# Optimization experiments

Hardware: AMD Instinct MI355X
Metric: run time of the kernel (lower is better)

Reference implementation:

```python
import jax, jax.numpy as jnp
import numpy as np

BS, QLEN, DIM, H = 2, 2048, 2048, 16
DH = DIM // H


def setup_inputs() -> dict:
    key = jax.random.key(0)
    ks = jax.random.split(key, 10)
    s = 0.02
    return {
        "input": jax.random.normal(ks[0], (BS, QLEN, DIM), jnp.float32),
        "mask": jnp.ones((BS, QLEN), jnp.int32),
        "wq": jax.random.normal(ks[1], (DIM, DIM), jnp.float32) * s,
        "bq": jax.random.normal(ks[2], (DIM,), jnp.float32) * s,
        "wk": jax.random.normal(ks[3], (DIM, DIM), jnp.float32) * s,
        "bk": jax.random.normal(ks[4], (DIM,), jnp.float32) * s,
        "wv": jax.random.normal(ks[5], (DIM, DIM), jnp.float32) * s,
        "bv": jax.random.normal(ks[6], (DIM,), jnp.float32) * s,
        "wo": jax.random.normal(ks[7], (DIM, DIM), jnp.float32) * s,
        "bo": jax.random.normal(ks[8], (DIM,), jnp.float32) * s,
    }


def _shape(x, bs):
    # (bs, len, dim) -> (bs, H, len, DH)
    return x.reshape(bs, -1, H, DH).transpose(0, 2, 1, 3)


def reference(input, mask, wq, bq, wk, bk, wv, bv, wo, bo):
    bs, qlen, dim = input.shape
    # torch Linear: y = x @ W.T + b
    q = _shape(input @ wq.T + bq, bs)  # (bs,H,q,dh)
    k = _shape(input @ wk.T + bk, bs)  # (bs,H,k,dh)
    v = _shape(input @ wv.T + bv, bs)  # (bs,H,k,dh)
    q = q / jnp.sqrt(jnp.asarray(DH, q.dtype))
    scores = jnp.einsum("bhqd,bhkd->bhqk", q, k)
    # mask (bs, klen): positions where mask==0 are masked with -inf
    neg = (mask == 0)[:, None, None, :]  # (bs,1,1,klen)
    scores = jnp.where(neg, -jnp.inf, scores)
    weights = jax.nn.softmax(scores.astype(jnp.float32), axis=-1).astype(scores.dtype)
    # dropout p=0 (eval): identity
    context = jnp.einsum("bhqk,bhkd->bhqd", weights, v)
    context = context.transpose(0, 2, 1, 3).reshape(bs, qlen, dim)
    return context @ wo.T + bo
```

## Files before the change

### kernel.cpp

```cpp
#include <hip/hip_runtime.h>
#include <hip/hip_bf16.h>

#define BS 2
#define QLEN 2048
#define DIM 2048
#define H 16
#define DH 128
#define MTOT (BS*QLEN)

typedef __hip_bfloat16 bf16;
using f32x4 = __attribute__((ext_vector_type(4))) float;
using s16x8 = __attribute__((ext_vector_type(8))) short;

__device__ inline void gload_lds16(const bf16* g, bf16* l) {
    __builtin_amdgcn_global_load_lds(
        (const __attribute__((address_space(1))) void*)g,
        (__attribute__((address_space(3))) void*)l,
        16, 0, 0);
}

__global__ __launch_bounds__(256) void cast6(
    const float* __restrict__ x,
    const float* __restrict__ w0, const float* __restrict__ w1,
    const float* __restrict__ w2, const float* __restrict__ w3,
    bf16* xo, bf16* o0, bf16* o1, bf16* o2, bf16* o3, int n4)
{
    const float* in; bf16* out;
    switch (blockIdx.y) {
        case 0:  in = w0; out = o0; break;
        case 1:  in = w1; out = o1; break;
        case 2:  in = w2; out = o2; break;
        case 3:  in = w3; out = o3; break;
        case 4:  in = x;        out = xo;        break;
        default: in = x + 4*(size_t)n4; out = xo + 4*(size_t)n4; break;
    }
    int i = blockIdx.x * 256 + threadIdx.x;
    if (i < n4) {
        float4 v = ((const float4*)in)[i];
        __hip_bfloat162 p0 = __float22bfloat162_rn(make_float2(v.x, v.y));
        __hip_bfloat162 p1 = __float22bfloat162_rn(make_float2(v.z, v.w));
        ((__hip_bfloat162*)out)[2*i]   = p0;
        ((__hip_bfloat162*)out)[2*i+1] = p1;
    }
}

__global__ __launch_bounds__(256) void gemm_qkv(
    const bf16* __restrict__ A,
    const bf16* __restrict__ Wq, const bf16* __restrict__ Wk, const bf16* __restrict__ Wv,
    const float* __restrict__ bq, const float* __restrict__ bk, const float* __restrict__ bv,
    bf16* __restrict__ Qo, bf16* __restrict__ Ko, bf16* __restrict__ Vo,
    float qscale)
{
    __shared__ __align__(16) bf16 smem[128*136];
    bf16* As = smem;
    bf16* Bs = smem + 128*64;

    const int z = blockIdx.z;
    const bf16*  B    = (z == 0) ? Wq : (z == 1) ? Wk : Wv;
    const float* bias = (z == 0) ? bq : (z == 1) ? bk : bv;
    const float  scale = (z == 0) ? qscale : 1.0f;

    const int t = threadIdx.x;
    const int lane = t & 63, w = t >> 6;
    const int row16 = lane & 15, quad = lane >> 4;
    const int m0 = blockIdx.y * 128, n0 = blockIdx.x * 128;
    const int mo = (w >> 1) * 64, no = (w & 1) * 64;

    f32x4 acc[4][4];
    for (int i = 0; i < 4; i++)
        for (int j = 0; j < 4; j++)
            acc[i][j] = (f32x4){0.f, 0.f, 0.f, 0.f};

    for (int kt = 0; kt < DIM; kt += 64) {
        __syncthreads();
        #pragma unroll
        for (int i = 0; i < 4; i++) {
            int idx = i*256 + t;
            int row = idx >> 3, g = idx & 7;
            int src = g ^ (row & 7);
            gload_lds16(A + (size_t)(m0 + row) * DIM + kt + src*8, &As[idx*8]);
            gload_lds16(B + (size_t)(n0 + row) * DIM + kt + src*8, &Bs[idx*8]);
        }
        __syncthreads();

        #pragma unroll
        for (int kh = 0; kh < 2; kh++) {
            s16x8 af[4], bfr[4];
            #pragma unroll
            for (int mt = 0; mt < 4; mt++)
                af[mt] = *(const s16x8*)&As[(mo + mt*16 + row16)*64 + (((kh*4+quad) ^ (row16&7)))*8];
            #pragma unroll
            for (int nt = 0; nt < 4; nt++)
                bfr[nt] = *(const s16x8*)&Bs[(no + nt*16 + row16)*64 + (((kh*4+quad) ^ (row16&7)))*8];
            #pragma unroll
            for (int mt = 0; mt < 4; mt++)
                #pragma unroll
                for (int nt = 0; nt < 4; nt++)
                    acc[mt][nt] = __builtin_amdgcn_mfma_f32_16x16x32_bf16(
                        af[mt], bfr[nt], acc[mt][nt], 0, 0, 0);
        }
    }

    if (z < 2) {
        bf16* out = (z == 0) ? Qo : Ko;
        for (int mt = 0; mt < 4; mt++)
            for (int nt = 0; nt < 4; nt++) {
                int n = n0 + no + nt*16 + row16;
                float bv_ = bias[n];
                for (int r = 0; r < 4; r++) {
                    int m = m0 + mo + mt*16 + quad*4 + r;
                    out[(size_t)m * DIM + n] = __float2bfloat16((acc[mt][nt][r] + bv_) * scale);
                }
            }
    } else {
        __syncthreads();
        bf16* Ts = smem;
        for (int mt = 0; mt < 4; mt++)
            for (int nt = 0; nt < 4; nt++) {
                int nn = no + nt*16 + row16;
                float bv_ = bias[n0 + nn];
                for (int r = 0; r < 4; r++) {
                    int mm = mo + mt*16 + quad*4 + r;
                    Ts[nn*136 + mm] = __float2bfloat16(acc[mt][nt][r] + bv_);
                }
            }
        __syncthreads();
        const int b = m0 >> 11, q0b = m0 & 2047;
        for (int i = 0; i < 8; i++) {
            int chunk = t + i*256;
            int row = chunk >> 4;
            int c16 = chunk & 15;
            s16x8 val = *(const s16x8*)&Ts[row*136 + c16*8];
            *(s16x8*)(Vo + ((size_t)(b*DIM + n0 + row))*QLEN + q0b + c16*8) = val;
        }
    }
}

__global__ __launch_bounds__(256) void gemm_out(
    const bf16* __restrict__ A, const bf16* __restrict__ B,
    const float* __restrict__ bias, float* __restrict__ out)
{
    __shared__ __align__(16) bf16 As[128*64];
    __shared__ __align__(16) bf16 Bs[128*64];

    const int t = threadIdx.x;
    const int lane = t & 63, w = t >> 6;
    const int row16 = lane & 15, quad = lane >> 4;
    const int m0 = blockIdx.y * 128, n0 = blockIdx.x * 128;
    const int mo = (w >> 1) * 64, no = (w & 1) * 64;

    f32x4 acc[4][4];
    for (int i = 0; i < 4; i++)
        for (int j = 0; j < 4; j++)
            acc[i][j] = (f32x4){0.f, 0.f, 0.f, 0.f};

    for (int kt = 0; kt < DIM; kt += 64) {
        __syncthreads();
        #pragma unroll
        for (int i = 0; i < 4; i++) {
            int idx = i*256 + t;
            int row = idx >> 3, g = idx & 7;
            int src = g ^ (row & 7);
            gload_lds16(A + (size_t)(m0 + row) * DIM + kt + src*8, &As[idx*8]);
            gload_lds16(B + (size_t)(n0 + row) * DIM + kt + src*8, &Bs[idx*8]);
        }
        __syncthreads();

        #pragma unroll
        for (int kh = 0; kh < 2; kh++) {
            s16x8 af[4], bfr[4];
            #pragma unroll
            for (int mt = 0; mt < 4; mt++)
                af[mt] = *(const s16x8*)&As[(mo + mt*16 + row16)*64 + (((kh*4+quad) ^ (row16&7)))*8];
            #pragma unroll
            for (int nt = 0; nt < 4; nt++)
                bfr[nt] = *(const s16x8*)&Bs[(no + nt*16 + row16)*64 + (((kh*4+quad) ^ (row16&7)))*8];
            #pragma unroll
            for (int mt = 0; mt < 4; mt++)
                #pragma unroll
                for (int nt = 0; nt < 4; nt++)
                    acc[mt][nt] = __builtin_amdgcn_mfma_f32_16x16x32_bf16(
                        af[mt], bfr[nt], acc[mt][nt], 0, 0, 0);
        }
    }

    for (int mt = 0; mt < 4; mt++)
        for (int nt = 0; nt < 4; nt++) {
            int n = n0 + no + nt*16 + row16;
            float bv_ = bias[n];
            for (int r = 0; r < 4; r++) {
                int m = m0 + mo + mt*16 + quad*4 + r;
                out[(size_t)m * DIM + n] = acc[mt][nt][r] + bv_;
            }
        }
}

__global__ __launch_bounds__(256, 2) void attn(
    const bf16* __restrict__ Q, const bf16* __restrict__ Kb,
    const bf16* __restrict__ Vt, const int* __restrict__ mask,
    bf16* __restrict__ Ctx)
{
    __shared__ __align__(16) bf16 Ks[2][64*128];
    __shared__ __align__(16) bf16 Vs[128*64];
    __shared__ __align__(16) bf16 Pl[4][32*64];

    const int t = threadIdx.x, w = t >> 6, lane = t & 63;
    const int row16 = lane & 15, quad = lane >> 4;
    const int bh = blockIdx.y, b = bh >> 4, h = bh & 15;
    const int q0 = blockIdx.x * 128 + w * 32;

    s16x8 qf[2][4];
    for (int qs = 0; qs < 2; qs++) {
        const bf16* qp = Q + (size_t)(b*QLEN + q0 + qs*16 + row16) * DIM + h*DH;
        for (int ks = 0; ks < 4; ks++)
            qf[qs][ks] = *(const s16x8*)(qp + ks*32 + quad*8);
    }

    f32x4 o[2][8];
    for (int qs = 0; qs < 2; qs++)
        for (int i = 0; i < 8; i++) o[qs][i] = (f32x4){0.f, 0.f, 0.f, 0.f};
    float lsum[2][4] = {{0.f,0.f,0.f,0.f},{0.f,0.f,0.f,0.f}};
    const int* mrow = mask + b * QLEN;

    const bf16* Kbase = Kb + (size_t)b*QLEN*DIM + h*DH;
    const bf16* Vbase = Vt + ((size_t)b*DIM + h*DH) * QLEN;

    #pragma unroll
    for (int i = 0; i < 4; i++) {
        int idx = i*256 + t;
        int kr = idx >> 4, kc = idx & 15;
        int kg = kc ^ (kr & 15);
        gload_lds16(Kbase + (size_t)kr * DIM + kg*8, &Ks[0][idx*8]);
    }

    for (int it = 0; it < QLEN/64; it++) {
        const int kt = it * 64, buf = it & 1;
        __syncthreads();

        if (it + 1 < QLEN/64) {
            #pragma unroll
            for (int i = 0; i < 4; i++) {
                int idx = i*256 + t;
                int kr = idx >> 4, kc = idx & 15;
                int kg = kc ^ (kr & 15);
                gload_lds16(Kbase + (size_t)(kt + 64 + kr) * DIM + kg*8, &Ks[buf^1][idx*8]);
            }
        }
        #pragma unroll
        for (int i = 0; i < 4; i++) {
            int idx = i*256 + t;
            int vd = idx >> 3, vc = idx & 7;
            int vg = vc ^ (vd & 7);
            gload_lds16(Vbase + (size_t)vd * QLEN + kt + vg*8, &Vs[idx*8]);
        }

        float mval[4];
        #pragma unroll
        for (int nt = 0; nt < 4; nt++)
            mval[nt] = (mrow[kt + nt*16 + row16] != 0) ? -20.0f : -1e30f;

        f32x4 sc[2][4];
        for (int qs = 0; qs < 2; qs++)
            for (int nt = 0; nt < 4; nt++) sc[qs][nt] = (f32x4){0.f, 0.f, 0.f, 0.f};
        #pragma unroll
        for (int ks = 0; ks < 4; ks++) {
            #pragma unroll
            for (int nt = 0; nt < 4; nt++) {
                int rrow = nt*16 + row16;
                int c = (ks*4 + quad) ^ row16;
                s16x8 kf = *(const s16x8*)&Ks[buf][rrow*128 + c*8];
                sc[0][nt] = __builtin_amdgcn_mfma_f32_16x16x32_bf16(qf[0][ks], kf, sc[0][nt], 0, 0, 0);
                sc[1][nt] = __builtin_amdgcn_mfma_f32_16x16x32_bf16(qf[1][ks], kf, sc[1][nt], 0, 0, 0);
            }
        }

        #pragma unroll
        for (int qs = 0; qs < 2; qs++) {
            #pragma unroll
            for (int r = 0; r < 4; r++) {
                int prow = qs*16 + quad*4 + r;
                float ts = 0.f;
                #pragma unroll
                for (int nt = 0; nt < 4; nt++) {
                    float p = exp2f(sc[qs][nt][r] + mval[nt]);
                    ts += p;
                    int chunk = nt*2 + (row16 >> 3);
                    int slot = chunk ^ (prow & 7);
                    Pl[w][prow*64 + slot*8 + (row16 & 7)] = __float2bfloat16(p);
                }
                lsum[qs][r] += ts;
            }
        }

        __syncthreads();

        #pragma unroll
        for (int kc = 0; kc < 2; kc++) {
            int pslot0 = ((kc*4 + quad) ^ (row16 & 7));
            s16x8 pf0 = *(const s16x8*)&Pl[w][(0*16 + row16)*64 + pslot0*8];
            s16x8 pf1 = *(const s16x8*)&Pl[w][(1*16 + row16)*64 + pslot0*8];
            #pragma unroll
            for (int nt = 0; nt < 8; nt++) {
                int d = nt*16 + row16;
                int c = (kc*4 + quad) ^ (d & 7);
                s16x8 vf = *(const s16x8*)&Vs[d*64 + c*8];
                o[0][nt] = __builtin_amdgcn_mfma_f32_16x16x32_bf16(pf0, vf, o[0][nt], 0, 0, 0);
                o[1][nt] = __builtin_amdgcn_mfma_f32_16x16x32_bf16(pf1, vf, o[1][nt], 0, 0, 0);
            }
        }
    }

    for (int qs = 0; qs < 2; qs++) {
        float inv[4];
        for (int r = 0; r < 4; r++) {
            float ts = lsum[qs][r];
            ts += __shfl_xor(ts, 1);
            ts += __shfl_xor(ts, 2);
            ts += __shfl_xor(ts, 4);
            ts += __shfl_xor(ts, 8);
            inv[r] = 1.0f / ts;
        }
        for (int nt = 0; nt < 8; nt++)
            for (int r = 0; r < 4; r++) {
                float v = o[qs][nt][r] * inv[r];
                Ctx[(size_t)(b*QLEN + q0 + qs*16 + quad*4 + r) * DIM + h*DH + nt*16 + row16] =
                    __float2bfloat16(v);
            }
    }
}

extern "C" void kernel_launch(void* const* d_in, const int* in_sizes, int n_in,
                              void* d_out, int out_size, void* d_ws, size_t ws_size,
                              hipStream_t stream) {
    const float* x    = (const float*)d_in[0];
    const int*   mask = (const int*)d_in[1];
    const float* wq   = (const float*)d_in[2];
    const float* bq   = (const float*)d_in[3];
    const float* wk   = (const float*)d_in[4];
    const float* bk   = (const float*)d_in[5];
    const float* wv   = (const float*)d_in[6];
    const float* bv   = (const float*)d_in[7];
    const float* wo   = (const float*)d_in[8];
    const float* bo   = (const float*)d_in[9];

    char* ws = (char*)d_ws;
    const size_t MB = 1024 * 1024;
    bf16* Xb  = (bf16*)(ws);
    bf16* Qb  = (bf16*)(ws + 16*MB);
    bf16* Kb  = (bf16*)(ws + 32*MB);
    bf16* Vtb = (bf16*)(ws + 48*MB);
    bf16* Wqb = (bf16*)(ws + 64*MB);
    bf16* Wkb = (bf16*)(ws + 72*MB);
    bf16* Wvb = (bf16*)(ws + 80*MB);
    bf16* Wob = (bf16*)(ws + 88*MB);
    bf16* Ctx = Xb;

    int n4w = (DIM*DIM) / 4;
    cast6<<<dim3(n4w/256, 6), 256, 0, stream>>>(x, wq, wk, wv, wo,
                                                Xb, Wqb, Wkb, Wvb, Wob, n4w);

    const float qscale = 0.08838834764831845f * 1.4426950408889634f;
    gemm_qkv<<<dim3(DIM/128, MTOT/128, 3), 256, 0, stream>>>(
        Xb, Wqb, Wkb, Wvb, bq, bk, bv, Qb, Kb, Vtb, qscale);

    attn<<<dim3(QLEN/128, BS*H), 256, 0, stream>>>(Qb, Kb, Vtb, mask, Ctx);

    gemm_out<<<dim3(DIM/128, MTOT/128), 256, 0, stream>>>(Ctx, Wob, bo, (float*)d_out);
}
```

Baseline: 416.1 us.

## Halve attention key tile, double-buffer V, drop mid-iteration barrier

```diff
diff --git a/kernel.cpp b/kernel.cpp
--- a/kernel.cpp
+++ b/kernel.cpp
@@ -195,14 +195,14 @@
         }
 }
 
-__global__ __launch_bounds__(256, 2) void attn(
+__global__ __launch_bounds__(256, 3) void attn(
     const bf16* __restrict__ Q, const bf16* __restrict__ Kb,
     const bf16* __restrict__ Vt, const int* __restrict__ mask,
     bf16* __restrict__ Ctx)
 {
-    __shared__ __align__(16) bf16 Ks[2][64*128];
-    __shared__ __align__(16) bf16 Vs[128*64];
-    __shared__ __align__(16) bf16 Pl[4][32*64];
+    __shared__ __align__(16) bf16 Ks[2][32*128];
+    __shared__ __align__(16) bf16 Vs[2][128*32];
+    __shared__ __align__(16) bf16 Pl[4][32*32];
 
     const int t = threadIdx.x, w = t >> 6, lane = t & 63;
     const int row16 = lane & 15, quad = lane >> 4;
@@ -226,49 +226,47 @@
     const bf16* Vbase = Vt + ((size_t)b*DIM + h*DH) * QLEN;
 
     #pragma unroll
-    for (int i = 0; i < 4; i++) {
+    for (int i = 0; i < 2; i++) {
         int idx = i*256 + t;
         int kr = idx >> 4, kc = idx & 15;
-        int kg = kc ^ (kr & 15);
-        gload_lds16(Kbase + (size_t)kr * DIM + kg*8, &Ks[0][idx*8]);
-    }
-
-    for (int it = 0; it < QLEN/64; it++) {
-        const int kt = it * 64, buf = it & 1;
-        __syncthreads();
-
-        if (it + 1 < QLEN/64) {
-            #pragma unroll
-            for (int i = 0; i < 4; i++) {
+        gload_lds16(Kbase + (size_t)kr * DIM + ((kc ^ (kr & 15)))*8, &Ks[0][idx*8]);
+        int vd = idx >> 2, vc = idx & 3;
+        gload_lds16(Vbase + (size_t)vd * QLEN + ((vc ^ (vd & 3)))*8, &Vs[0][idx*8]);
+    }
+
+    for (int it = 0; it < QLEN/32; it++) {
+        const int kt = it * 32, buf = it & 1;
+        __syncthreads();
+
+        if (it + 1 < QLEN/32) {
+            const int kt2 = kt + 32;
+            #pragma unroll
+            for (int i = 0; i < 2; i++) {
                 int idx = i*256 + t;
                 int kr = idx >> 4, kc = idx & 15;
-                int kg = kc ^ (kr & 15);
-                gload_lds16(Kbase + (size_t)(kt + 64 + kr) * DIM + kg*8, &Ks[buf^1][idx*8]);
-            }
-        }
-        #pragma unroll
-        for (int i = 0; i < 4; i++) {
-            int idx = i*256 + t;
-            int vd = idx >> 3, vc = idx & 7;
-            int vg = vc ^ (vd & 7);
-            gload_lds16(Vbase + (size_t)vd * QLEN + kt + vg*8, &Vs[idx*8]);
-        }
-
-        float mval[4];
-        #pragma unroll
-        for (int nt = 0; nt < 4; nt++)
+                gload_lds16(Kbase + (size_t)(kt2 + kr) * DIM + ((kc ^ (kr & 15)))*8,
+                            &Ks[buf^1][idx*8]);
+                int vd = idx >> 2, vc = idx & 3;
+                gload_lds16(Vbase + (size_t)vd * QLEN + kt2 + ((vc ^ (vd & 3)))*8,
+                            &Vs[buf^1][idx*8]);
+            }
+        }
+
+        float mval[2];
+        #pragma unroll
+        for (int nt = 0; nt < 2; nt++)
             mval[nt] = (mrow[kt + nt*16 + row16] != 0) ? -20.0f : -1e30f;
 
-        f32x4 sc[2][4];
+        f32x4 sc[2][2];
         for (int qs = 0; qs < 2; qs++)
-            for (int nt = 0; nt < 4; nt++) sc[qs][nt] = (f32x4){0.f, 0.f, 0.f, 0.f};
+            for (int nt = 0; nt < 2; nt++) sc[qs][nt] = (f32x4){0.f, 0.f, 0.f, 0.f};
         #pragma unroll
         for (int ks = 0; ks < 4; ks++) {
             #pragma unroll
-            for (int nt = 0; nt < 4; nt++) {
+            for (int nt = 0; nt < 2; nt++) {
                 int rrow = nt*16 + row16;
-                int c = (ks*4 + quad) ^ row16;
-                s16x8 kf = *(const s16x8*)&Ks[buf][rrow*128 + c*8];
+                int slot = (ks*4 + quad) ^ (rrow & 15);
+                s16x8 kf = *(const s16x8*)&Ks[buf][rrow*128 + slot*8];
                 sc[0][nt] = __builtin_amdgcn_mfma_f32_16x16x32_bf16(qf[0][ks], kf, sc[0][nt], 0, 0, 0);
                 sc[1][nt] = __builtin_amdgcn_mfma_f32_16x16x32_bf16(qf[1][ks], kf, sc[1][nt], 0, 0, 0);
             }
@@ -279,31 +277,30 @@
             #pragma unroll
             for (int r = 0; r < 4; r++) {
                 int prow = qs*16 + quad*4 + r;
+                int swz = (qs*4 + quad) & 3;
                 float ts = 0.f;
                 #pragma unroll
-                for (int nt = 0; nt < 4; nt++) {
+                for (int nt = 0; nt < 2; nt++) {
                     float p = exp2f(sc[qs][nt][r] + mval[nt]);
                     ts += p;
                     int chunk = nt*2 + (row16 >> 3);
-                    int slot = chunk ^ (prow & 7);
-                    Pl[w][prow*64 + slot*8 + (row16 & 7)] = __float2bfloat16(p);
+                    int slot = chunk ^ swz;
+                    Pl[w][prow*32 + slot*8 + (row16 & 7)] = __float2bfloat16(p);
                 }
                 lsum[qs][r] += ts;
             }
         }
 
-        __syncthreads();
-
-        #pragma unroll
-        for (int kc = 0; kc < 2; kc++) {
-            int pslot0 = ((kc*4 + quad) ^ (row16 & 7));
-            s16x8 pf0 = *(const s16x8*)&Pl[w][(0*16 + row16)*64 + pslot0*8];
-            s16x8 pf1 = *(const s16x8*)&Pl[w][(1*16 + row16)*64 + pslot0*8];
+        {
+            int ps0 = quad ^ ((0*4 + (row16 >> 2)) & 3);
+            int ps1 = quad ^ ((1*4 + (row16 >> 2)) & 3);
+            s16x8 pf0 = *(const s16x8*)&Pl[w][(0*16 + row16)*32 + ps0*8];
+            s16x8 pf1 = *(const s16x8*)&Pl[w][(1*16 + row16)*32 + ps1*8];
             #pragma unroll
             for (int nt = 0; nt < 8; nt++) {
                 int d = nt*16 + row16;
-                int c = (kc*4 + quad) ^ (d & 7);
-                s16x8 vf = *(const s16x8*)&Vs[d*64 + c*8];
+                int vslot = quad ^ (d & 3);
+                s16x8 vf = *(const s16x8*)&Vs[buf][d*32 + vslot*8];
                 o[0][nt] = __builtin_amdgcn_mfma_f32_16x16x32_bf16(pf0, vf, o[0][nt], 0, 0, 0);
                 o[1][nt] = __builtin_amdgcn_mfma_f32_16x16x32_bf16(pf1, vf, o[1][nt], 0, 0, 0);
             }
```

After: 439.0 us. +5.5%, slower.
